# Optimization experiments

Hardware: AMD Instinct MI355X
Metric: run time of the kernel (lower is better)

Reference implementation:

```python
import jax, jax.numpy as jnp
import numpy as np
from jax import lax

STRIDE = 4
RADII = (0.1, 0.2)
NSAMPLES = (16, 32)


def fps(xyz, npoint):
    """Iterative farthest point sampling. xyz: (B,N,3) -> idx (B,npoint) int32."""
    B, N, _ = xyz.shape

    def body(carry, _):
        dists, last = carry  # (B,N), (B,)
        last_pt = jnp.take_along_axis(xyz, last[:, None, None], axis=1)  # (B,1,3)
        d = jnp.sum((xyz - last_pt) ** 2, axis=-1)  # (B,N)
        dists = jnp.minimum(dists, d)
        nxt = jnp.argmax(dists, axis=-1).astype(jnp.int32)
        return (dists, nxt), last

    init = (jnp.full((B, N), 1e10, xyz.dtype), jnp.zeros((B,), jnp.int32))
    _, idxs = lax.scan(body, init, None, length=npoint)
    return jnp.transpose(idxs)  # (B, npoint)


def ball_query(radius, nsample, support_xyz, query_xyz):
    """First-nsample-in-ball neighbor indices, padded with the first valid index.
    Returns idx (B,S,K) int32."""
    N = support_xyz.shape[1]
    d2 = (jnp.sum(query_xyz ** 2, -1, keepdims=True)
          + jnp.sum(support_xyz ** 2, -1)[:, None, :]
          - 2.0 * jnp.einsum('bsd,bnd->bsn', query_xyz, support_xyz))  # (B,S,N)
    in_ball = d2 <= radius * radius
    key = jnp.where(in_ball, jnp.arange(N, dtype=jnp.int32), N)  # smallest index first
    neg_key, idx = lax.top_k(-key, nsample)  # smallest keys
    valid = (-neg_key) < N
    idx = jnp.where(valid, idx, idx[..., :1])  # pad empty slots with first neighbor
    return idx


def gather_points(pts, idx):
    """pts (B,N,D), idx (B,S,K) -> (B,S,K,D)"""
    B, S, K = idx.shape
    D = pts.shape[-1]
    out = jnp.take_along_axis(pts, idx.reshape(B, S * K, 1), axis=1)
    return out.reshape(B, S, K, D)


def scale_block(query_xyz, support_xyz, feats_t, radius, nsample, weights):
    idx = ball_query(radius, nsample, support_xyz, query_xyz)
    g_xyz = gather_points(support_xyz, idx) - query_xyz[:, :, None, :]  # relative coords
    g_feat = gather_points(feats_t, idx)
    h = jnp.concatenate([g_xyz, g_feat], axis=-1)  # (B,S,K,3+C)
    for W, b in weights:  # shared pointwise MLP (1x1 conv) + ReLU
        h = jax.nn.relu(jnp.einsum('bskc,cd->bskd', h, W) + b)
    return jnp.max(h, axis=2)  # max-pool over neighbors -> (B,S,Cout)


def setup_inputs() -> dict:
    key = jax.random.key(0)
    ks = jax.random.split(key, 10)
    B, N, C = 8, 8192, 64
    inp = {
        'support_xyz': jax.random.uniform(ks[0], (B, N, 3), jnp.float32),
        'support_features': jax.random.normal(ks[1], (B, C, N), jnp.float32),
    }
    dims0 = [(67, 64), (64, 64), (64, 128)]
    dims1 = [(67, 64), (64, 96), (96, 128)]
    k = 2
    for s, dims in ((0, dims0), (1, dims1)):
        for j, (din, dout) in enumerate(dims):
            inp[f's{s}_w{j}'] = jax.random.normal(ks[k], (din, dout), jnp.float32) * 0.02
            inp[f's{s}_b{j}'] = jnp.zeros((dout,), jnp.float32)
            k += 1
    return inp


def reference(support_xyz, support_features,
              s0_w0, s0_b0, s0_w1, s0_b1, s0_w2, s0_b2,
              s1_w0, s1_b0, s1_w1, s1_b1, s1_w2, s1_b2):
    B, N, _ = support_xyz.shape
    npoint = N // STRIDE
    idx = fps(support_xyz, npoint)  # (B,npoint)
    query_xyz = jnp.take_along_axis(support_xyz, idx[:, :, None], axis=1)  # (B,npoint,3)
    feats_t = jnp.transpose(support_features, (0, 2, 1))  # (B,N,C)
    w0 = [(s0_w0, s0_b0), (s0_w1, s0_b1), (s0_w2, s0_b2)]
    w1 = [(s1_w0, s1_b0), (s1_w1, s1_b1), (s1_w2, s1_b2)]
    f0 = scale_block(query_xyz, support_xyz, feats_t, RADII[0], NSAMPLES[0], w0)
    f1 = scale_block(query_xyz, support_xyz, feats_t, RADII[1], NSAMPLES[1], w1)
    new_features = jnp.transpose(jnp.concatenate([f0, f1], axis=-1), (0, 2, 1))  # (B,256,npoint)
    return query_xyz, new_features
```

## Files before the change

### kernel.cpp

```cpp
#include <hip/hip_runtime.h>

#define N_SUP 8192
#define N_QPT 2048
#define SMEM_BYTES 121360
#define UNIT_LDS 60672
#define N_CHUNKS 12288

typedef float v2f __attribute__((ext_vector_type(2)));

__device__ __forceinline__ float sumsq3(float x, float y, float z) {
#pragma clang fp contract(off)
  return x * x + y * y + z * z;
}

__device__ __forceinline__ float dot3(float ax, float ay, float az,
                                      float bx, float by, float bz) {
#pragma clang fp contract(off)
  return ax * bx + ay * by + az * bz;
}

__device__ __forceinline__ float d2_expand(float A, float Bn, float d) {
#pragma clang fp contract(off)
  return (A + Bn) - 2.0f * d;
}

template <int CTRL>
__device__ __forceinline__ unsigned long long dppmax64(unsigned long long k) {
  unsigned lo = (unsigned)k, hi = (unsigned)(k >> 32);
  unsigned olo =
      (unsigned)__builtin_amdgcn_update_dpp((int)lo, (int)lo, CTRL, 0xf, 0xf, false);
  unsigned ohi =
      (unsigned)__builtin_amdgcn_update_dpp((int)hi, (int)hi, CTRL, 0xf, 0xf, false);
  unsigned long long o = (((unsigned long long)ohi) << 32) | olo;
  return (o > k) ? o : k;
}

__device__ __forceinline__ unsigned long long wavemax_u64(unsigned long long k) {
  k = dppmax64<0x111>(k);
  k = dppmax64<0x112>(k);
  k = dppmax64<0x114>(k);
  k = dppmax64<0x118>(k);
  k = dppmax64<0x142>(k);
  k = dppmax64<0x143>(k);
  return k;
}

__global__ __launch_bounds__(256) void prep_xyz_kernel(
    const float* __restrict__ xyz, float* __restrict__ xs,
    float* __restrict__ ys, float* __restrict__ zs, float* __restrict__ bsq,
    int* __restrict__ flags) {
  int p = blockIdx.x * 256 + threadIdx.x;
  float x = xyz[p * 3 + 0];
  float y = xyz[p * 3 + 1];
  float z = xyz[p * 3 + 2];
  xs[p] = x; ys[p] = y; zs[p] = z;
  bsq[p] = sumsq3(x, y, z);
  if (blockIdx.x == 0) {
    flags[threadIdx.x] = 0;
    if (threadIdx.x < 64) flags[256 + threadIdx.x] = 0;
  }
}

__global__ __launch_bounds__(256) void transpose_feats_kernel(
    const float* __restrict__ feats, float* __restrict__ fT) {
  __shared__ float tile[64][65];
  int b = blockIdx.x >> 7;
  int nb = (blockIdx.x & 127) << 6;
  int t = threadIdx.x;
#pragma unroll
  for (int i = 0; i < 16; ++i) {
    int e = i * 256 + t;
    int c = e >> 6, n = e & 63;
    tile[n][c] = feats[(b * 64 + c) * N_SUP + nb + n];
  }
  __syncthreads();
#pragma unroll
  for (int i = 0; i < 16; ++i) {
    int e = i * 256 + t;
    int n = e >> 6, c = e & 63;
    fT[(b * N_SUP + nb + n) * 64 + c] = tile[n][c];
  }
}

__device__ __forceinline__ void bq_wave(int lane, const float* __restrict__ sx,
                                        const float* __restrict__ sy,
                                        const float* __restrict__ sz,
                                        const float* __restrict__ sq, float qx,
                                        float qy, float qz, float r2, int K,
                                        int* __restrict__ out) {
  const float A = sumsq3(qx, qy, qz);
  int cnt = 0, first = 0;
  const unsigned long long ltmask = (1ull << lane) - 1ull;
  for (int base = 0; base < N_SUP; base += 64) {
    int n = base + lane;
    float d = dot3(qx, qy, qz, sx[n], sy[n], sz[n]);
    float d2 = d2_expand(A, sq[n], d);
    bool in = d2 <= r2;
    unsigned long long m = __ballot(in);
    if (in) {
      int pos = cnt + __popcll(m & ltmask);
      if (pos < K) out[pos] = n;
    }
    if (cnt == 0 && m != 0ull) first = base + __ffsll((long long)m) - 1;
    cnt += __popcll(m);
    if (cnt >= K) break;
  }
  for (int p = cnt + lane; p < K; p += 64) out[p] = first;
}

template <int CIN, int SIN, int D, int SOUT>
__device__ __forceinline__ void dense_layer(const float* __restrict__ hin,
                                            float* __restrict__ hout,
                                            const float* __restrict__ W,
                                            const float* __restrict__ Bv,
                                            int w, int lane) {
  constexpr int CH = D / 16;
#pragma unroll
  for (int pass = 0; pass * 4 < CH; ++pass) {
    const int chunk = pass * 4 + w;
    if (chunk < CH) {
      const int co = chunk * 16;
      float acc[16];
#pragma unroll
      for (int j = 0; j < 16; ++j) acc[j] = Bv[co + j];
      const float* hr = hin + lane * SIN;
      const float* wp = W + co;
#pragma unroll 4
      for (int c = 0; c < CIN; ++c) {
        float a = hr[c];
#pragma unroll
        for (int j = 0; j < 16; ++j) acc[j] = fmaf(a, wp[c * D + j], acc[j]);
      }
      float* ho = hout + lane * SOUT + co;
#pragma unroll
      for (int j = 0; j < 16; ++j) ho[j] = fmaxf(acc[j], 0.0f);
    }
  }
}

template <int K, int Q, int C2, int S2, int CHOFF>
__device__ __forceinline__ void consumer_body(
    int tl, int qg0, float r2, char* um, const float* __restrict__ xs,
    const float* __restrict__ ys, const float* __restrict__ zs,
    const float* __restrict__ bsq, const float* __restrict__ fT, float* qxyz,
    int* prog, const float* __restrict__ W1, const float* __restrict__ B1,
    const float* __restrict__ W2, const float* __restrict__ B2,
    const float* __restrict__ W3, const float* __restrict__ B3,
    float* __restrict__ outf) {
  constexpr int S0 = 67, S1 = 65;
  float* smem = (float*)um;
  int* lidx = (int*)(um + 41472);
  float* qc = (float*)(um + 41728);
  float* h1 = smem;
  float* h0 = smem + 64 * S1;
  float* h2 = h0;
  const int w = __builtin_amdgcn_readfirstlane(tl >> 6);
  const int lane = tl & 63;
  const int b = qg0 >> 11;
  const int need = (qg0 & 2047) + Q;
  int* pp = prog + b * 32;
  while (__hip_atomic_load(pp, __ATOMIC_RELAXED, __HIP_MEMORY_SCOPE_AGENT) <
         need)
    __builtin_amdgcn_s_sleep(32);
  if (tl < Q * 3)
    qc[tl] = __hip_atomic_load(&qxyz[qg0 * 3 + tl], __ATOMIC_RELAXED,
                               __HIP_MEMORY_SCOPE_AGENT);
  __syncthreads();
  if (w < Q)
    bq_wave(lane, xs + b * N_SUP, ys + b * N_SUP, zs + b * N_SUP,
            bsq + b * N_SUP, qc[w * 3], qc[w * 3 + 1], qc[w * 3 + 2], r2, K,
            lidx + w * K);
  __syncthreads();
#pragma unroll
  for (int e = tl; e < 64 * S0; e += 256) {
    int r = e / S0, c2 = e - r * S0;
    int qi = r / K, k = r - qi * K;
    int n = lidx[qi * K + k];
    float v;
    if (c2 < 3) {
      const float* sp = (c2 == 0) ? xs : (c2 == 1) ? ys : zs;
      v = sp[b * N_SUP + n] - qc[qi * 3 + c2];
    } else {
      v = fT[(b * N_SUP + n) * 64 + (c2 - 3)];
    }
    h0[e] = v;
  }
  __syncthreads();
  dense_layer<67, S0, 64, S1>(h0, h1, W1, B1, w, lane);
  __syncthreads();
  dense_layer<64, S1, C2, S2>(h1, h2, W2, B2, w, lane);
  __syncthreads();
#pragma unroll
  for (int pass = 0; pass < 2; ++pass) {
    const int co = (pass * 4 + w) * 16;
    float acc[16];
#pragma unroll
    for (int j = 0; j < 16; ++j) acc[j] = B3[co + j];
    const float* hr = h2 + lane * S2;
#pragma unroll 4
    for (int c = 0; c < C2; ++c) {
      float a = hr[c];
#pragma unroll
      for (int j = 0; j < 16; ++j)
        acc[j] = fmaf(a, W3[c * 128 + co + j], acc[j]);
    }
#pragma unroll
    for (int j = 0; j < 16; ++j) acc[j] = fmaxf(acc[j], 0.0f);
#pragma unroll
    for (int off = K / 2; off >= 1; off >>= 1) {
#pragma unroll
      for (int j = 0; j < 16; ++j)
        acc[j] = fmaxf(acc[j], __shfl_xor(acc[j], off));
    }
    if ((lane & (K - 1)) == 0) {
      int qg = qg0 + (lane / K);
      int bo = qg >> 11, s = qg & 2047;
      float* dst = outf + ((bo * 256 + CHOFF + co) * 2048 + s);
#pragma unroll
      for (int j = 0; j < 16; ++j) dst[j * 2048] = acc[j];
    }
  }
}

__device__ void fps_producer(const float* __restrict__ xs,
                             const float* __restrict__ ys,
                             const float* __restrict__ zs, float* qxyz,
                             int* prog, char* smraw) {
  const int b = blockIdx.x;
  const int t = threadIdx.x;
  float* sxL = (float*)smraw;
  float* syL = (float*)(smraw + 32768);
  float* szL = (float*)(smraw + 65536);
  unsigned short* sorig = (unsigned short*)(smraw + 98304);
  unsigned* hist = (unsigned*)(smraw + 114688);
  unsigned* offs = (unsigned*)(smraw + 116736);
  unsigned* cursor = (unsigned*)(smraw + 118784);
  unsigned long long* skey = (unsigned long long*)(smraw + 120832);
  const float* bx = xs + b * N_SUP;
  const float* by = ys + b * N_SUP;
  const float* bz = zs + b * N_SUP;

  hist[t] = 0u;
  __syncthreads();
  for (int j = 0; j < 16; ++j) {
    int n = t + j * 512;
    float x = bx[n], y = by[n], z = bz[n];
    int cx = min(7, (int)(x * 8.0f));
    int cy = min(7, (int)(y * 8.0f));
    int cz = min(7, (int)(z * 8.0f));
    atomicAdd(&hist[(cx << 6) | (cy << 3) | cz], 1u);
  }
  __syncthreads();
  offs[t] = hist[t];
  __syncthreads();
  for (int d = 1; d < 512; d <<= 1) {
    unsigned v = (t >= d) ? offs[t - d] : 0u;
    __syncthreads();
    offs[t] += v;
    __syncthreads();
  }
  cursor[t] = offs[t] - hist[t];
  __syncthreads();
  for (int j = 0; j < 16; ++j) {
    int n = t + j * 512;
    float x = bx[n], y = by[n], z = bz[n];
    int cx = min(7, (int)(x * 8.0f));
    int cy = min(7, (int)(y * 8.0f));
    int cz = min(7, (int)(z * 8.0f));
    unsigned pos = atomicAdd(&cursor[(cx << 6) | (cy << 3) | cz], 1u);
    sxL[pos] = x; syL[pos] = y; szL[pos] = z;
    sorig[pos] = (unsigned short)n;
  }
  __syncthreads();

  v2f px[8], py[8], pz[8], dm[8];
  unsigned payx[8], payy[8];
  const int base = t * 16;
#pragma unroll
  for (int j = 0; j < 8; ++j) {
    int p0 = base + 2 * j, p1 = p0 + 1;
    px[j] = (v2f){sxL[p0], sxL[p1]};
    py[j] = (v2f){syL[p0], syL[p1]};
    pz[j] = (v2f){szL[p0], szL[p1]};
    payx[j] = ((unsigned)(N_SUP - 1 - sorig[p0]) << 13) | (unsigned)p0;
    payy[j] = ((unsigned)(N_SUP - 1 - sorig[p1]) << 13) | (unsigned)p1;
    dm[j] = (v2f){1e10f, 1e10f};
  }
  float lox = px[0].x, hix = px[0].x;
  float loy = py[0].x, hiy = py[0].x;
  float loz = pz[0].x, hiz = pz[0].x;
#pragma unroll
  for (int j = 0; j < 8; ++j) {
    lox = fminf(lox, fminf(px[j].x, px[j].y));
    hix = fmaxf(hix, fmaxf(px[j].x, px[j].y));
    loy = fminf(loy, fminf(py[j].x, py[j].y));
    hiy = fmaxf(hiy, fmaxf(py[j].x, py[j].y));
    loz = fminf(loz, fminf(pz[j].x, pz[j].y));
    hiz = fmaxf(hiz, fmaxf(pz[j].x, pz[j].y));
  }
  float tval = 1e10f;
  unsigned long long tkey = 0ull, wkey = 0ull;
  float lxp = bx[0], lyp = by[0], lzp = bz[0];
  float* q = qxyz + b * N_QPT * 3;
  if (t == 0) { q[0] = lxp; q[1] = lyp; q[2] = lzp; }
  const int wv = t >> 6;
  const bool is63 = (t & 63) == 63;

  for (int it = 1; it < N_QPT; ++it) {
    float dxl = fmaxf(fmaxf(lox - lxp, lxp - hix), 0.0f);
    float dyl = fmaxf(fmaxf(loy - lyp, lyp - hiy), 0.0f);
    float dzl = fmaxf(fmaxf(loz - lzp, lzp - hiz), 0.0f);
    float db2 = dxl * dxl + dyl * dyl + dzl * dzl;
    bool dirty = db2 < tval * 1.0001f + 1e-12f;
    if (__ballot(dirty)) {
      if (dirty) {
        float nx = -lxp, ny = -lyp, nz = -lzp;
        v2f nx2 = (v2f){nx, nx}, ny2 = (v2f){ny, ny}, nz2 = (v2f){nz, nz};
        float lm = -1.0f;
#pragma unroll
        for (int j = 0; j < 8; ++j) {
#pragma clang fp contract(off)
          v2f dx = px[j] + nx2;
          v2f dy = py[j] + ny2;
          v2f dz = pz[j] + nz2;
          v2f s = dx * dx + dy * dy;
          s = s + dz * dz;
          v2f nd = __builtin_elementwise_min(dm[j], s);
          dm[j] = nd;
          lm = fmaxf(lm, fmaxf(nd.x, nd.y));
        }
        tval = lm;
        unsigned pay = 0u;
#pragma unroll
        for (int j = 0; j < 8; ++j) {
          if (dm[j].x == tval) pay = max(pay, payx[j]);
          if (dm[j].y == tval) pay = max(pay, payy[j]);
        }
        tkey = (((unsigned long long)__float_as_uint(tval)) << 32) | pay;
      }
      wkey = wavemax_u64(tkey);
    }
    if (is63) skey[(it & 1) * 8 + wv] = wkey;
    __syncthreads();
    const ulonglong2* pk = (const ulonglong2*)(skey + (it & 1) * 8);
    ulonglong2 A = pk[0], B = pk[1], C = pk[2], D = pk[3];
    unsigned long long k0 = (A.y > A.x) ? A.y : A.x;
    unsigned long long k1 = (B.y > B.x) ? B.y : B.x;
    unsigned long long k2 = (C.y > C.x) ? C.y : C.x;
    unsigned long long k3 = (D.y > D.x) ? D.y : D.x;
    k0 = (k1 > k0) ? k1 : k0;
    k2 = (k3 > k2) ? k3 : k2;
    k0 = (k2 > k0) ? k2 : k0;
    unsigned pos = (unsigned)k0 & 0x1FFFu;
    lxp = sxL[pos]; lyp = syL[pos]; lzp = szL[pos];
    if (t == 0) {
      q[it * 3 + 0] = lxp;
      q[it * 3 + 1] = lyp;
      q[it * 3 + 2] = lzp;
      if ((it & 63) == 63)
        __hip_atomic_store(prog + b * 32, it + 1, __ATOMIC_RELEASE,
                           __HIP_MEMORY_SCOPE_AGENT);
    }
  }
  __syncthreads();
}

__global__ __launch_bounds__(512) void fused_kernel(
    const float* __restrict__ xs, const float* __restrict__ ys,
    const float* __restrict__ zs, const float* __restrict__ bsq,
    const float* __restrict__ fT, float* qxyz, float* outf, int* prog,
    int* qwork, const float* W10, const float* B10, const float* W11,
    const float* B11, const float* W12, const float* B12, const float* W20,
    const float* B20, const float* W21, const float* B21, const float* W22,
    const float* B22) {
  __shared__ __align__(16) char smraw[SMEM_BYTES];
  if (blockIdx.x < 8) {
    fps_producer(xs, ys, zs, qxyz, prog, smraw);
  }
  const int t = threadIdx.x;
  const int unit = t >> 8;
  const int tl = t & 255;
  char* um = smraw + unit * UNIT_LDS;
  int* lch = (int*)(smraw + 121344);
  for (;;) {
    if (t == 0) {
      int c0 = atomicAdd(qwork, 2);
      lch[0] = c0;
      lch[1] = c0 + 1;
    }
    __syncthreads();
    int c = lch[unit];
    if (lch[0] >= N_CHUNKS) return;
    if (c < N_CHUNKS) {
      int g = c / 3, r = c - g * 3;
      if (r == 0) {
        int qg0 = ((g & 7) << 11) + ((g >> 3) << 2);
        consumer_body<16, 4, 64, 65, 0>(tl, qg0, 0.01f, um, xs, ys, zs, bsq,
                                        fT, qxyz, prog, W10, B10, W11, B11,
                                        W12, B12, outf);
      } else {
        int h = 2 * g + r - 1;
        int qg0 = (((h >> 1) & 7) << 11) + ((h >> 4) << 2) + ((h & 1) << 1);
        consumer_body<32, 2, 96, 97, 128>(tl, qg0, 0.04f, um, xs, ys, zs, bsq,
                                          fT, qxyz, prog, W20, B20, W21, B21,
                                          W22, B22, outf);
      }
    } else {
      __syncthreads();
      __syncthreads();
      __syncthreads();
      __syncthreads();
      __syncthreads();
    }
  }
}

extern "C" void kernel_launch(void* const* d_in, const int* in_sizes, int n_in,
                              void* d_out, int out_size, void* d_ws,
                              size_t ws_size, hipStream_t stream) {
  const float* xyz = (const float*)d_in[0];
  const float* feats = (const float*)d_in[1];
  const float* wt[12];
  for (int i = 0; i < 12; ++i) wt[i] = (const float*)d_in[2 + i];

  float* ws = (float*)d_ws;
  float* xs = ws;
  float* ys = ws + 65536;
  float* zs = ws + 131072;
  float* bsq = ws + 196608;
  float* fT = ws + 262144;
  int* flags = (int*)(ws + 4456448);
  int* prog = flags;
  int* qwork = flags + 256;

  float* qxyz = (float*)d_out;
  float* outf = qxyz + 8 * 2048 * 3;

  prep_xyz_kernel<<<dim3(256), dim3(256), 0, stream>>>(xyz, xs, ys, zs, bsq,
                                                       flags);
  transpose_feats_kernel<<<dim3(1024), dim3(256), 0, stream>>>(feats, fT);
  fused_kernel<<<dim3(256), dim3(512), 0, stream>>>(
      xs, ys, zs, bsq, fT, qxyz, outf, prog, qwork, wt[0], wt[1], wt[2], wt[3],
      wt[4], wt[5], wt[6], wt[7], wt[8], wt[9], wt[10], wt[11]);
}
```

Measured before the change: 2.647 ms.

## Run three consumer units per block and vectorize ball query and gather loads

Blocks grow from 512 to 768 threads, so three 256-thread consumer units now share LDS, made possible by shrinking per-unit LDS. Each work fetch grabs three chunks instead of two. The FPS producer masks out the extra threads. The ball query now reads float4 (four points per lane per step), and the feature gather uses float4 loads from the transposed features. The aim is more concurrent consumers and fewer memory instructions, at the cost of register pressure under the 768-thread launch bound and a possible slowdown of the FPS producer, which is the critical path.

```diff
diff --git a/kernel.cpp b/kernel.cpp
--- a/kernel.cpp
+++ b/kernel.cpp
@@ -2,8 +2,8 @@
 
 #define N_SUP 8192
 #define N_QPT 2048
-#define SMEM_BYTES 121360
-#define UNIT_LDS 60672
+#define UNIT_LDS 41792
+#define SMEM_BYTES 125440
 #define N_CHUNKS 12288
 
 typedef float v2f __attribute__((ext_vector_type(2)));
@@ -82,27 +82,48 @@
   }
 }
 
-__device__ __forceinline__ void bq_wave(int lane, const float* __restrict__ sx,
-                                        const float* __restrict__ sy,
-                                        const float* __restrict__ sz,
-                                        const float* __restrict__ sq, float qx,
-                                        float qy, float qz, float r2, int K,
-                                        int* __restrict__ out) {
+__device__ __forceinline__ void bq_wave4(int lane, const float* __restrict__ sx,
+                                         const float* __restrict__ sy,
+                                         const float* __restrict__ sz,
+                                         const float* __restrict__ sq,
+                                         float qx, float qy, float qz,
+                                         float r2, int K,
+                                         int* __restrict__ out) {
   const float A = sumsq3(qx, qy, qz);
   int cnt = 0, first = 0;
-  const unsigned long long ltmask = (1ull << lane) - 1ull;
-  for (int base = 0; base < N_SUP; base += 64) {
-    int n = base + lane;
-    float d = dot3(qx, qy, qz, sx[n], sy[n], sz[n]);
-    float d2 = d2_expand(A, sq[n], d);
-    bool in = d2 <= r2;
-    unsigned long long m = __ballot(in);
-    if (in) {
-      int pos = cnt + __popcll(m & ltmask);
-      if (pos < K) out[pos] = n;
-    }
-    if (cnt == 0 && m != 0ull) first = base + __ffsll((long long)m) - 1;
-    cnt += __popcll(m);
+  const unsigned long long lt = (1ull << lane) - 1ull;
+  for (int base = 0; base < N_SUP; base += 256) {
+    float4 x4 = ((const float4*)(sx + base))[lane];
+    float4 y4 = ((const float4*)(sy + base))[lane];
+    float4 z4 = ((const float4*)(sz + base))[lane];
+    float4 q4 = ((const float4*)(sq + base))[lane];
+    float da = d2_expand(A, q4.x, dot3(qx, qy, qz, x4.x, y4.x, z4.x));
+    float db = d2_expand(A, q4.y, dot3(qx, qy, qz, x4.y, y4.y, z4.y));
+    float dc = d2_expand(A, q4.z, dot3(qx, qy, qz, x4.z, y4.z, z4.z));
+    float dd = d2_expand(A, q4.w, dot3(qx, qy, qz, x4.w, y4.w, z4.w));
+    bool i0 = da <= r2, i1 = db <= r2, i2 = dc <= r2, i3 = dd <= r2;
+    unsigned long long M0 = __ballot(i0), M1 = __ballot(i1);
+    unsigned long long M2 = __ballot(i2), M3 = __ballot(i3);
+    int below = __popcll(M0 & lt) + __popcll(M1 & lt) + __popcll(M2 & lt) +
+                __popcll(M3 & lt);
+    int p0 = cnt + below;
+    int p1 = p0 + (i0 ? 1 : 0);
+    int p2 = p1 + (i1 ? 1 : 0);
+    int p3 = p2 + (i2 ? 1 : 0);
+    int nb = base + 4 * lane;
+    if (i0 && p0 < K) out[p0] = nb;
+    if (i1 && p1 < K) out[p1] = nb + 1;
+    if (i2 && p2 < K) out[p2] = nb + 2;
+    if (i3 && p3 < K) out[p3] = nb + 3;
+    if (cnt == 0) {
+      unsigned mn = 0xFFFFFFFFu;
+      if (M0) mn = min(mn, (unsigned)(4 * (__ffsll((long long)M0) - 1)));
+      if (M1) mn = min(mn, (unsigned)(4 * (__ffsll((long long)M1) - 1) + 1));
+      if (M2) mn = min(mn, (unsigned)(4 * (__ffsll((long long)M2) - 1) + 2));
+      if (M3) mn = min(mn, (unsigned)(4 * (__ffsll((long long)M3) - 1) + 3));
+      if (mn != 0xFFFFFFFFu) first = base + (int)mn;
+    }
+    cnt += __popcll(M0) + __popcll(M1) + __popcll(M2) + __popcll(M3);
     if (cnt >= K) break;
   }
   for (int p = cnt + lane; p < K; p += 64) out[p] = first;
@@ -167,23 +188,25 @@
                                __HIP_MEMORY_SCOPE_AGENT);
   __syncthreads();
   if (w < Q)
-    bq_wave(lane, xs + b * N_SUP, ys + b * N_SUP, zs + b * N_SUP,
-            bsq + b * N_SUP, qc[w * 3], qc[w * 3 + 1], qc[w * 3 + 2], r2, K,
-            lidx + w * K);
-  __syncthreads();
-#pragma unroll
-  for (int e = tl; e < 64 * S0; e += 256) {
-    int r = e / S0, c2 = e - r * S0;
-    int qi = r / K, k = r - qi * K;
-    int n = lidx[qi * K + k];
-    float v;
-    if (c2 < 3) {
-      const float* sp = (c2 == 0) ? xs : (c2 == 1) ? ys : zs;
-      v = sp[b * N_SUP + n] - qc[qi * 3 + c2];
-    } else {
-      v = fT[(b * N_SUP + n) * 64 + (c2 - 3)];
-    }
-    h0[e] = v;
+    bq_wave4(lane, xs + b * N_SUP, ys + b * N_SUP, zs + b * N_SUP,
+             bsq + b * N_SUP, qc[w * 3], qc[w * 3 + 1], qc[w * 3 + 2], r2, K,
+             lidx + w * K);
+  __syncthreads();
+  if (tl < 192) {
+    int r = tl / 3, c2 = tl - r * 3;
+    int qi = r / K;
+    int n = lidx[r];
+    const float* sp = (c2 == 0) ? xs : (c2 == 1) ? ys : zs;
+    h0[r * S0 + c2] = sp[b * N_SUP + n] - qc[qi * 3 + c2];
+  }
+#pragma unroll
+  for (int i = 0; i < 4; ++i) {
+    int idx = tl + 256 * i;
+    int r = idx >> 4, fi = idx & 15;
+    int n = lidx[r];
+    float4 v = ((const float4*)(fT + (size_t)(b * N_SUP + n) * 64))[fi];
+    float* d = h0 + r * S0 + 3 + 4 * fi;
+    d[0] = v.x; d[1] = v.y; d[2] = v.z; d[3] = v.w;
   }
   __syncthreads();
   dense_layer<67, S0, 64, S1>(h0, h1, W1, B1, w, lane);
@@ -228,6 +251,7 @@
                              int* prog, char* smraw) {
   const int b = blockIdx.x;
   const int t = threadIdx.x;
+  const bool act = t < 512;
   float* sxL = (float*)smraw;
   float* syL = (float*)(smraw + 32768);
   float* szL = (float*)(smraw + 65536);
@@ -240,63 +264,71 @@
   const float* by = ys + b * N_SUP;
   const float* bz = zs + b * N_SUP;
 
-  hist[t] = 0u;
-  __syncthreads();
-  for (int j = 0; j < 16; ++j) {
-    int n = t + j * 512;
-    float x = bx[n], y = by[n], z = bz[n];
-    int cx = min(7, (int)(x * 8.0f));
-    int cy = min(7, (int)(y * 8.0f));
-    int cz = min(7, (int)(z * 8.0f));
-    atomicAdd(&hist[(cx << 6) | (cy << 3) | cz], 1u);
-  }
-  __syncthreads();
-  offs[t] = hist[t];
+  if (act) hist[t] = 0u;
+  __syncthreads();
+  if (act) {
+    for (int j = 0; j < 16; ++j) {
+      int n = t + j * 512;
+      float x = bx[n], y = by[n], z = bz[n];
+      int cx = min(7, (int)(x * 8.0f));
+      int cy = min(7, (int)(y * 8.0f));
+      int cz = min(7, (int)(z * 8.0f));
+      atomicAdd(&hist[(cx << 6) | (cy << 3) | cz], 1u);
+    }
+  }
+  __syncthreads();
+  if (act) offs[t] = hist[t];
   __syncthreads();
   for (int d = 1; d < 512; d <<= 1) {
-    unsigned v = (t >= d) ? offs[t - d] : 0u;
+    unsigned v = 0;
+    if (act && t >= d) v = offs[t - d];
     __syncthreads();
-    offs[t] += v;
+    if (act) offs[t] += v;
     __syncthreads();
   }
-  cursor[t] = offs[t] - hist[t];
-  __syncthreads();
-  for (int j = 0; j < 16; ++j) {
-    int n = t + j * 512;
-    float x = bx[n], y = by[n], z = bz[n];
-    int cx = min(7, (int)(x * 8.0f));
-    int cy = min(7, (int)(y * 8.0f));
-    int cz = min(7, (int)(z * 8.0f));
-    unsigned pos = atomicAdd(&cursor[(cx << 6) | (cy << 3) | cz], 1u);
-    sxL[pos] = x; syL[pos] = y; szL[pos] = z;
-    sorig[pos] = (unsigned short)n;
+  if (act) cursor[t] = offs[t] - hist[t];
+  __syncthreads();
+  if (act) {
+    for (int j = 0; j < 16; ++j) {
+      int n = t + j * 512;
+      float x = bx[n], y = by[n], z = bz[n];
+      int cx = min(7, (int)(x * 8.0f));
+      int cy = min(7, (int)(y * 8.0f));
+      int cz = min(7, (int)(z * 8.0f));
+      unsigned pos = atomicAdd(&cursor[(cx << 6) | (cy << 3) | cz], 1u);
+      sxL[pos] = x; syL[pos] = y; szL[pos] = z;
+      sorig[pos] = (unsigned short)n;
+    }
   }
   __syncthreads();
 
   v2f px[8], py[8], pz[8], dm[8];
   unsigned payx[8], payy[8];
-  const int base = t * 16;
-#pragma unroll
-  for (int j = 0; j < 8; ++j) {
-    int p0 = base + 2 * j, p1 = p0 + 1;
-    px[j] = (v2f){sxL[p0], sxL[p1]};
-    py[j] = (v2f){syL[p0], syL[p1]};
-    pz[j] = (v2f){szL[p0], szL[p1]};
-    payx[j] = ((unsigned)(N_SUP - 1 - sorig[p0]) << 13) | (unsigned)p0;
-    payy[j] = ((unsigned)(N_SUP - 1 - sorig[p1]) << 13) | (unsigned)p1;
-    dm[j] = (v2f){1e10f, 1e10f};
-  }
-  float lox = px[0].x, hix = px[0].x;
-  float loy = py[0].x, hiy = py[0].x;
-  float loz = pz[0].x, hiz = pz[0].x;
-#pragma unroll
-  for (int j = 0; j < 8; ++j) {
-    lox = fminf(lox, fminf(px[j].x, px[j].y));
-    hix = fmaxf(hix, fmaxf(px[j].x, px[j].y));
-    loy = fminf(loy, fminf(py[j].x, py[j].y));
-    hiy = fmaxf(hiy, fmaxf(py[j].x, py[j].y));
-    loz = fminf(loz, fminf(pz[j].x, pz[j].y));
-    hiz = fmaxf(hiz, fmaxf(pz[j].x, pz[j].y));
+  float lox = 0, hix = 0, loy = 0, hiy = 0, loz = 0, hiz = 0;
+  if (act) {
+    const int base = t * 16;
+#pragma unroll
+    for (int j = 0; j < 8; ++j) {
+      int p0 = base + 2 * j, p1 = p0 + 1;
+      px[j] = (v2f){sxL[p0], sxL[p1]};
+      py[j] = (v2f){syL[p0], syL[p1]};
+      pz[j] = (v2f){szL[p0], szL[p1]};
+      payx[j] = ((unsigned)(N_SUP - 1 - sorig[p0]) << 13) | (unsigned)p0;
+      payy[j] = ((unsigned)(N_SUP - 1 - sorig[p1]) << 13) | (unsigned)p1;
+      dm[j] = (v2f){1e10f, 1e10f};
+    }
+    lox = hix = px[0].x;
+    loy = hiy = py[0].x;
+    loz = hiz = pz[0].x;
+#pragma unroll
+    for (int j = 0; j < 8; ++j) {
+      lox = fminf(lox, fminf(px[j].x, px[j].y));
+      hix = fmaxf(hix, fmaxf(px[j].x, px[j].y));
+      loy = fminf(loy, fminf(py[j].x, py[j].y));
+      hiy = fmaxf(hiy, fmaxf(py[j].x, py[j].y));
+      loz = fminf(loz, fminf(pz[j].x, pz[j].y));
+      hiz = fmaxf(hiz, fmaxf(pz[j].x, pz[j].y));
+    }
   }
   float tval = 1e10f;
   unsigned long long tkey = 0ull, wkey = 0ull;
@@ -304,14 +336,17 @@
   float* q = qxyz + b * N_QPT * 3;
   if (t == 0) { q[0] = lxp; q[1] = lyp; q[2] = lzp; }
   const int wv = t >> 6;
-  const bool is63 = (t & 63) == 63;
+  const bool is63 = ((t & 63) == 63) && act;
 
   for (int it = 1; it < N_QPT; ++it) {
-    float dxl = fmaxf(fmaxf(lox - lxp, lxp - hix), 0.0f);
-    float dyl = fmaxf(fmaxf(loy - lyp, lyp - hiy), 0.0f);
-    float dzl = fmaxf(fmaxf(loz - lzp, lzp - hiz), 0.0f);
-    float db2 = dxl * dxl + dyl * dyl + dzl * dzl;
-    bool dirty = db2 < tval * 1.0001f + 1e-12f;
+    bool dirty = false;
+    if (act) {
+      float dxl = fmaxf(fmaxf(lox - lxp, lxp - hix), 0.0f);
+      float dyl = fmaxf(fmaxf(loy - lyp, lyp - hiy), 0.0f);
+      float dzl = fmaxf(fmaxf(loz - lzp, lzp - hiz), 0.0f);
+      float db2 = dxl * dxl + dyl * dyl + dzl * dzl;
+      dirty = db2 < tval * 1.0001f + 1e-12f;
+    }
     if (__ballot(dirty)) {
       if (dirty) {
         float nx = -lxp, ny = -lyp, nz = -lzp;
@@ -365,7 +400,7 @@
   __syncthreads();
 }
 
-__global__ __launch_bounds__(512) void fused_kernel(
+__global__ __launch_bounds__(768) void fused_kernel(
     const float* __restrict__ xs, const float* __restrict__ ys,
     const float* __restrict__ zs, const float* __restrict__ bsq,
     const float* __restrict__ fT, float* qxyz, float* outf, int* prog,
@@ -381,12 +416,13 @@
   const int unit = t >> 8;
   const int tl = t & 255;
   char* um = smraw + unit * UNIT_LDS;
-  int* lch = (int*)(smraw + 121344);
+  int* lch = (int*)(smraw + 3 * UNIT_LDS);
   for (;;) {
     if (t == 0) {
-      int c0 = atomicAdd(qwork, 2);
+      int c0 = atomicAdd(qwork, 3);
       lch[0] = c0;
       lch[1] = c0 + 1;
+      lch[2] = c0 + 2;
     }
     __syncthreads();
     int c = lch[unit];
@@ -439,7 +475,7 @@
   prep_xyz_kernel<<<dim3(256), dim3(256), 0, stream>>>(xyz, xs, ys, zs, bsq,
                                                        flags);
   transpose_feats_kernel<<<dim3(1024), dim3(256), 0, stream>>>(feats, fT);
-  fused_kernel<<<dim3(256), dim3(512), 0, stream>>>(
+  fused_kernel<<<dim3(256), dim3(768), 0, stream>>>(
       xs, ys, zs, bsq, fT, qxyz, outf, prog, qwork, wt[0], wt[1], wt[2], wt[3],
       wt[4], wt[5], wt[6], wt[7], wt[8], wt[9], wt[10], wt[11]);
 }
```

Result: faster. 2.272 ms, median of 2 (-14.2%).
